# Kernel tuning notes

Measured on AMD Instinct MI355X. Metric: run time of the kernel, lower is better.

## Reference

```python
import jax, jax.numpy as jnp
import numpy as np

NUM_BINS_X = 1024
NUM_BINS_Y = 1024
XL, XH, YL, YH = 0.0, 1024.0, 0.0, 1024.0
NUM_NODES = 4_000_000
NUM_FILLER = 1_000_000
NUM_PHYS = NUM_NODES - NUM_FILLER      # physical = movable + fixed
NUM_MOVABLE = 2_500_000
UNIT_PIN_CAPACITY = 2.0                # pins per unit area capacity
PIN_STRETCH_RATIO = 1.414              # DREAMPlace default sqrt(2)
MAX_ADJ = 2.5
MIN_ADJ = 1.0 / MAX_ADJ
SPAN = 4                               # max bins any box spans per axis (sizes <= 2*bin)


def setup_inputs() -> dict:
    key = jax.random.key(0)
    k1, k2, k3, k4, k5 = jax.random.split(key, 5)
    node_size_x = 0.5 + 1.5 * jax.random.uniform(k1, (NUM_NODES,), jnp.float32)
    node_size_y = 0.5 + 1.5 * jax.random.uniform(k2, (NUM_NODES,), jnp.float32)
    pos_x = XL + jax.random.uniform(k3, (NUM_NODES,), jnp.float32) * (XH - XL - 2.0)
    pos_y = YL + jax.random.uniform(k4, (NUM_NODES,), jnp.float32) * (YH - YL - 2.0)
    pos = jnp.concatenate([pos_x, pos_y])  # [2*num_nodes], x then y
    pin_weights = jax.random.randint(k5, (NUM_PHYS,), 1, 9, jnp.int32)
    return {"pos": pos, "node_size_x": node_size_x, "node_size_y": node_size_y,
            "pin_weights": pin_weights}


def _overlap(lo, hi, bin_lo, bin_size):
    # overlap length of interval [lo,hi] with bin [bin_lo, bin_lo+bin_size]
    return jnp.clip(jnp.minimum(hi, bin_lo + bin_size) - jnp.maximum(lo, bin_lo), 0.0, None)


def reference(pos, node_size_x, node_size_y, pin_weights):
    bsx = (XH - XL) / NUM_BINS_X
    bsy = (YH - YL) / NUM_BINS_Y
    dtype = pos.dtype

    # ---- phase 1: pin density map over stretched boxes of physical nodes ----
    sx = node_size_x[:NUM_PHYS]
    sy = node_size_y[:NUM_PHYS]
    hx = 0.5 * jnp.maximum(bsx * PIN_STRETCH_RATIO, sx)  # half stretched extent
    hy = 0.5 * jnp.maximum(bsy * PIN_STRETCH_RATIO, sy)
    cx = pos[:NUM_PHYS] + 0.5 * sx
    cy = pos[NUM_NODES:NUM_NODES + NUM_PHYS] + 0.5 * sy
    xmin, xmax = cx - hx, cx + hx
    ymin, ymax = cy - hy, cy + hy
    dens = pin_weights.astype(dtype) / (4.0 * hx * hy)   # pins per unit area

    bxl = jnp.clip(jnp.floor((xmin - XL) / bsx).astype(jnp.int32), 0, NUM_BINS_X - 1)
    byl = jnp.clip(jnp.floor((ymin - YL) / bsy).astype(jnp.int32), 0, NUM_BINS_Y - 1)

    pmap = jnp.zeros(NUM_BINS_X * NUM_BINS_Y, dtype)
    for di in range(SPAN):
        bx = bxl + di
        ox = _overlap(xmin, xmax, XL + bx.astype(dtype) * bsx, bsx)
        vx = bx < NUM_BINS_X
        for dj in range(SPAN):
            by = byl + dj
            oy = _overlap(ymin, ymax, YL + by.astype(dtype) * bsy, bsy)
            v = vx & (by < NUM_BINS_Y)
            idx = jnp.where(v, bx * NUM_BINS_Y + by, 0)
            val = jnp.where(v, dens * ox * oy, 0.0)
            pmap = pmap.at[idx].add(val)

    # density -> utilization: scatter added pins*overlap/area, divide by bin area
    pmap = pmap / (bsx * bsy)
    adj = jnp.clip(pmap / UNIT_PIN_CAPACITY, MIN_ADJ, MAX_ADJ)

    # ---- phase 2: per-movable-node pin-optimized area over actual footprint ----
    mx = pos[:NUM_MOVABLE]
    my = pos[NUM_NODES:NUM_NODES + NUM_MOVABLE]
    msx = node_size_x[:NUM_MOVABLE]
    msy = node_size_y[:NUM_MOVABLE]
    bxl2 = jnp.clip(jnp.floor((mx - XL) / bsx).astype(jnp.int32), 0, NUM_BINS_X - 1)
    byl2 = jnp.clip(jnp.floor((my - YL) / bsy).astype(jnp.int32), 0, NUM_BINS_Y - 1)

    area = jnp.zeros(NUM_MOVABLE, dtype)
    for di in range(SPAN):
        bx = bxl2 + di
        ox = _overlap(mx, mx + msx, XL + bx.astype(dtype) * bsx, bsx)
        vx = bx < NUM_BINS_X
        for dj in range(SPAN):
            by = byl2 + dj
            oy = _overlap(my, my + msy, YL + by.astype(dtype) * bsy, bsy)
            v = vx & (by < NUM_BINS_Y)
            idx = jnp.where(v, bx * NUM_BINS_Y + by, 0)
            area = area + jnp.where(v, ox * oy * adj[idx], 0.0)
    return area
```

## Files before the change

### kernel.cpp

```cpp
#include <hip/hip_runtime.h>

#define NBX 1024
#define NBY 1024
#define TS 64
#define NTX (NBX / TS)
#define NTY (NBY / TS)
#define NTILES (NTX * NTY)
#define LW 66
#define LSTRIDE 67
#define CAP 13056
#define CAPM 11008

#define FB_BLOCK 512
#define FB_K 8
#define FB_CHUNK (FB_BLOCK * FB_K)

#define SPLIT 2

#define PMAP_SCALE 131072.0f
#define PMAP_INV   (1.0f / 131072.0f)

static constexpr int NUM_NODES   = 4000000;
static constexpr int NUM_PHYS    = 3000000;
static constexpr int NUM_MOVABLE = 2500000;
static constexpr int HALF_MOV    = NUM_MOVABLE / 2;

typedef unsigned long long u64;

static constexpr size_t OFF_PMAP  = 0;
static constexpr size_t OFF_CURS  = OFF_PMAP + (size_t)NBX * NBY * 4;
static constexpr size_t OFF_CURSM = OFF_CURS + NTILES * 4;
static constexpr size_t OFF_SLAB  = ((OFF_CURSM + NTILES * 4 + 15) / 16) * 16;
static constexpr size_t OFF_MSLAB = ((OFF_SLAB + (size_t)NTILES * CAP * 8 + 15) / 16) * 16;
static constexpr size_t WS_FULL   = OFF_MSLAB + (size_t)NTILES * CAPM * 12;

__global__ void __launch_bounds__(FB_BLOCK)
fill_both(const float* __restrict__ pos, const float* __restrict__ nsx,
          const float* __restrict__ nsy, const int* __restrict__ pw,
          unsigned* __restrict__ curs, unsigned* __restrict__ cursm,
          uint2* __restrict__ slab, uint3* __restrict__ mslab) {
    __shared__ unsigned cntp[NTILES], cntm[NTILES];
    __shared__ unsigned offp[NTILES], offm[NTILES];
    __shared__ unsigned Dp[NTILES], Dm[NTILES];
    __shared__ unsigned wsum[8];
    __shared__ uint2 SAB[FB_CHUNK];
    __shared__ unsigned SC[FB_CHUNK];
    __shared__ unsigned short ST[FB_CHUNK];

    const int tid = threadIdx.x;
    const int b0  = blockIdx.x * FB_CHUNK;

    if (tid < NTILES) { cntp[tid] = 0u; cntm[tid] = 0u; }
    __syncthreads();

    u64 P[FB_K];
    u64 M[FB_K];
    int TPM[FB_K];
    unsigned rkP[FB_K], rkM[FB_K];

    #pragma unroll
    for (int k = 0; k < FB_K; ++k) {
        int i = b0 + k * FB_BLOCK + tid;
        int tp = -1, tm = -1;
        if (i < NUM_PHYS) {
            float mx = pos[i], my = pos[NUM_NODES + i];
            float sx = nsx[i], sy = nsy[i];
            float hx = 0.5f * fmaxf(1.414f, sx);
            float hy = 0.5f * fmaxf(1.414f, sy);
            unsigned qhx = (unsigned)__float2int_rn((hx - 0.7f) * 1024.0f);
            unsigned qhy = (unsigned)__float2int_rn((hy - 0.7f) * 1024.0f);
            float hxd = 0.7f + (float)qhx * (1.0f / 1024.0f);
            float hyd = 0.7f + (float)qhy * (1.0f / 1024.0f);
            float xmin = mx + 0.5f * sx - hxd;
            float ymin = my + 0.5f * sy - hyd;
            int bxl = min(max((int)floorf(xmin), 0), NBX - 1);
            int byl = min(max((int)floorf(ymin), 0), NBY - 1);
            tp = (bxl >> 6) * NTY + (byl >> 6);
            int bx0 = (tp >> 4) << 6, by0 = (tp & 15) << 6;
            unsigned ex = (unsigned)__float2int_rn((xmin - (float)bx0 + 1.0f) * 8192.0f);
            unsigned ey = (unsigned)__float2int_rn((ymin - (float)by0 + 1.0f) * 8192.0f);
            P[k] = (u64)ex | ((u64)ey << 20) | ((u64)qhx << 40)
                 | ((u64)qhy << 50) | ((u64)(unsigned)(pw[i] - 1) << 60);
            rkP[k] = atomicAdd(&cntp[tp], 1u);
            if (i < NUM_MOVABLE) {
                int bxm = min(max((int)floorf(mx), 0), NBX - 1);
                int bym = min(max((int)floorf(my), 0), NBY - 1);
                tm = (bxm >> 6) * NTY + (bym >> 6);
                int bx0m = (tm >> 4) << 6, by0m = (tm & 15) << 6;
                unsigned exm = (unsigned)__float2int_rn((mx - (float)bx0m) * 8192.0f);
                unsigned eym = (unsigned)__float2int_rn((my - (float)by0m) * 8192.0f);
                unsigned qsx = (unsigned)__float2int_rn((sx - 0.5f) * 2048.0f);
                unsigned qsy = (unsigned)__float2int_rn((sy - 0.5f) * 2048.0f);
                M[k] = (u64)exm | ((u64)eym << 20) | ((u64)qsx << 40) | ((u64)qsy << 52);
                rkM[k] = atomicAdd(&cntm[tm], 1u);
            }
        }
        TPM[k] = (tp & 0xffff) | (tm << 16);
    }
    __syncthreads();

    {
        const int lane   = tid & 63;
        const int scanId = tid & 255;
        const bool isMov = tid >= 256;
        unsigned* cnt = isMov ? cntm : cntp;
        unsigned* off = isMov ? offm : offp;
        unsigned* D   = isMov ? Dm : Dp;
        unsigned* gc  = isMov ? cursm : curs;

        unsigned v = cnt[scanId];
        unsigned x = v;
        #pragma unroll
        for (int d = 1; d < 64; d <<= 1) {
            unsigned y = __shfl_up(x, d);
            if (lane >= d) x += y;
        }
        if (lane == 63) wsum[tid >> 6] = x;
        __syncthreads();
        unsigned add = 0;
        const int w0  = isMov ? 4 : 0;
        const int myw = scanId >> 6;
        for (int w = 0; w < myw; ++w) add += wsum[w0 + w];
        unsigned o = x + add - v;
        unsigned base = v ? atomicAdd(&gc[scanId], v) : 0u;
        off[scanId] = o;
        D[scanId]   = base - o;
    }
    __syncthreads();

    #pragma unroll
    for (int k = 0; k < FB_K; ++k) {
        int tp = (int)(short)(TPM[k] & 0xffff);
        if (tp >= 0) {
            unsigned s = offp[tp] + rkP[k];
            SAB[s] = make_uint2((unsigned)P[k], (unsigned)(P[k] >> 32));
            ST[s]  = (unsigned short)tp;
        }
    }
    __syncthreads();

    {
        unsigned totP = offp[NTILES - 1] + cntp[NTILES - 1];
        for (unsigned j = tid; j < totP; j += FB_BLOCK) {
            unsigned tile = ST[j];
            unsigned p = Dp[tile] + j;
            if (p < CAP)
                slab[(size_t)tile * CAP + p] = SAB[j];
        }
    }
    __syncthreads();

    #pragma unroll
    for (int k = 0; k < FB_K; ++k) {
        int tm = TPM[k] >> 16;
        if (tm >= 0) {
            unsigned s = offm[tm] + rkM[k];
            SAB[s] = make_uint2((unsigned)M[k], (unsigned)(M[k] >> 32));
            SC[s]  = (unsigned)(b0 + k * FB_BLOCK + tid);
            ST[s]  = (unsigned short)tm;
        }
    }
    __syncthreads();

    {
        unsigned totM = offm[NTILES - 1] + cntm[NTILES - 1];
        for (unsigned j = tid; j < totM; j += FB_BLOCK) {
            unsigned tile = ST[j];
            unsigned p = Dm[tile] + j;
            if (p < CAPM) {
                uint2 ab = SAB[j];
                mslab[(size_t)tile * CAPM + p] = make_uint3(ab.x, ab.y, SC[j]);
            }
        }
    }
}

__global__ void __launch_bounds__(1024)
tile_scatter(const uint2* __restrict__ slab, const unsigned* __restrict__ curs,
             float* __restrict__ pmap) {
    __shared__ unsigned lds[LW * LSTRIDE];
    int t   = blockIdx.x / SPLIT;
    int sub = blockIdx.x - t * SPLIT;
    int bx0 = (t >> 4) << 6, by0 = (t & 15) << 6;

    for (int c = threadIdx.x; c < LW * LSTRIDE; c += 1024) lds[c] = 0u;
    __syncthreads();

    unsigned n = min(curs[t], (unsigned)CAP);
    const uint2* sl = slab + (size_t)t * CAP;

    unsigned k = threadIdx.x + sub * 1024;
    uint2 p = (k < n) ? sl[k] : make_uint2(0u, 0u);
    while (k < n) {
        unsigned kn = k + SPLIT * 1024;
        uint2 pn = (kn < n) ? sl[kn] : make_uint2(0u, 0u);

        u64 P = (u64)p.x | ((u64)p.y << 32);
        float xminl = (float)(P & 0xFFFFFu)         * (1.0f / 8192.0f) - 1.0f;
        float yminl = (float)((P >> 20) & 0xFFFFFu) * (1.0f / 8192.0f) - 1.0f;
        float hx = 0.7f + (float)((P >> 40) & 0x3FFu) * (1.0f / 1024.0f);
        float hy = 0.7f + (float)((P >> 50) & 0x3FFu) * (1.0f / 1024.0f);
        float pwv  = (float)(1u + (unsigned)(P >> 60));
        float dens = pwv / (4.0f * hx * hy);
        float xmaxl = xminl + 2.0f * hx;
        float ymaxl = yminl + 2.0f * hy;

        int lx0 = min(max((int)floorf(xminl), 0), TS - 1);
        int ly0 = min(max((int)floorf(yminl), 0), TS - 1);
        #pragma unroll
        for (int di = 0; di < 3; ++di) {
            float bl = (float)(lx0 + di);
            float ox = fminf(xmaxl, bl + 1.0f) - fmaxf(xminl, bl);
            if (ox <= 0.0f) continue;
            float dox = dens * ox;
            #pragma unroll
            for (int dj = 0; dj < 3; ++dj) {
                float bly = (float)(ly0 + dj);
                float oy  = fminf(ymaxl, bly + 1.0f) - fmaxf(yminl, bly);
                if (oy > 0.0f) {
                    unsigned q = (unsigned)__float2int_rn(dox * oy * PMAP_SCALE);
                    atomicAdd(&lds[(lx0 + di) * LSTRIDE + (ly0 + dj)], q);
                }
            }
        }
        p = pn;
        k = kn;
    }
    __syncthreads();

    for (int c = threadIdx.x; c < LW * LW; c += 1024) {
        int lx = c / LW, ly = c - lx * LW;
        int bx = bx0 + lx, by = by0 + ly;
        if (bx >= NBX || by >= NBY) continue;
        float v = (float)lds[lx * LSTRIDE + ly] * PMAP_INV;
        if (v != 0.0f)
            atomicAdd(&pmap[bx * NBY + by], v);
    }
}

__global__ void __launch_bounds__(1024)
gather_tile(const uint3* __restrict__ mslab, const unsigned* __restrict__ cursm,
            const float* __restrict__ pmap, float* __restrict__ out) {
    __shared__ float adj[LW * LSTRIDE];
    int t   = blockIdx.x / SPLIT;
    int sub = blockIdx.x - t * SPLIT;
    int bx0 = (t >> 4) << 6, by0 = (t & 15) << 6;

    for (int c = threadIdx.x; c < LW * LW; c += 1024) {
        int r = c / LW, col = c - r * LW;
        int bx = min(bx0 + r,  NBX - 1);
        int by = min(by0 + col, NBY - 1);
        adj[r * LSTRIDE + col] =
            fminf(fmaxf(pmap[bx * NBY + by] * 0.5f, 0.4f), 2.5f);
    }
    __syncthreads();

    unsigned n = min(cursm[t], (unsigned)CAPM);
    const uint3* sl = mslab + (size_t)t * CAPM;

    for (unsigned k = threadIdx.x + sub * 1024; k < n; k += SPLIT * 1024) {
        uint3 p = sl[k];
        u64 M = (u64)p.x | ((u64)p.y << 32);
        float mxl = (float)(M & 0xFFFFFu)         * (1.0f / 8192.0f);
        float myl = (float)((M >> 20) & 0xFFFFFu) * (1.0f / 8192.0f);
        float sx  = 0.5f + (float)((M >> 40) & 0xFFFu) * (1.0f / 2048.0f);
        float sy  = 0.5f + (float)(M >> 52)            * (1.0f / 2048.0f);
        float xmaxl = mxl + sx;
        float ymaxl = myl + sy;

        int lx0 = min((int)mxl, TS - 1);
        int ly0 = min((int)myl, TS - 1);

        float area = 0.0f;
        #pragma unroll
        for (int di = 0; di < 3; ++di) {
            float bl = (float)(lx0 + di);
            float ox = fmaxf(fminf(xmaxl, bl + 1.0f) - fmaxf(mxl, bl), 0.0f);
            #pragma unroll
            for (int dj = 0; dj < 3; ++dj) {
                float bly = (float)(ly0 + dj);
                float oy  = fmaxf(fminf(ymaxl, bly + 1.0f) - fmaxf(myl, bly), 0.0f);
                area += ox * oy * adj[(lx0 + di) * LSTRIDE + (ly0 + dj)];
            }
        }
        out[p.z] = area;
    }
}

__global__ void __launch_bounds__(256)
scatter_pin(const float* __restrict__ pos, const float* __restrict__ nsx,
            const float* __restrict__ nsy, const int* __restrict__ pw,
            float* __restrict__ pmap) {
    int i = blockIdx.x * blockDim.x + threadIdx.x;
    if (i >= NUM_PHYS) return;
    float sx = nsx[i], sy = nsy[i];
    float hx = 0.5f * fmaxf(1.414f, sx);
    float hy = 0.5f * fmaxf(1.414f, sy);
    float cx = pos[i] + 0.5f * sx;
    float cy = pos[NUM_NODES + i] + 0.5f * sy;
    float xmin = cx - hx, xmax = cx + hx;
    float ymin = cy - hy, ymax = cy + hy;
    float dens = (float)pw[i] / (4.0f * hx * hy);
    int bxl = min(max((int)floorf(xmin), 0), NBX - 1);
    int byl = min(max((int)floorf(ymin), 0), NBY - 1);
    #pragma unroll
    for (int di = 0; di < 3; ++di) {
        float bl = (float)(bxl + di);
        float ox = fminf(xmax, bl + 1.0f) - fmaxf(xmin, bl);
        if (ox <= 0.0f) continue;
        float dox = dens * ox;
        int base = min(bxl + di, NBX - 1) * NBY;
        #pragma unroll
        for (int dj = 0; dj < 3; ++dj) {
            float bly = (float)(byl + dj);
            float oy  = fminf(ymax, bly + 1.0f) - fmaxf(ymin, bly);
            if (oy > 0.0f) atomicAdd(&pmap[base + min(byl + dj, NBY - 1)], dox * oy);
        }
    }
}

__device__ __forceinline__ float gather_one(const float* __restrict__ pos,
                                            const float* __restrict__ nsx,
                                            const float* __restrict__ nsy,
                                            const float* __restrict__ pmap,
                                            int i) {
    float mx = pos[i];
    float my = pos[NUM_NODES + i];
    float xmax = mx + nsx[i];
    float ymax = my + nsy[i];
    int bxl = min(max((int)floorf(mx), 0), NBX - 1);
    int byl = min(max((int)floorf(my), 0), NBY - 1);
    float ox[3], oy[3];
    int rowb[3], colb[3];
    #pragma unroll
    for (int d = 0; d < 3; ++d) {
        float bl  = (float)(bxl + d);
        float bly = (float)(byl + d);
        ox[d] = fmaxf(fminf(xmax, bl + 1.0f) - fmaxf(mx, bl), 0.0f);
        oy[d] = fmaxf(fminf(ymax, bly + 1.0f) - fmaxf(my, bly), 0.0f);
        rowb[d] = min(bxl + d, NBX - 1) * NBY;
        colb[d] = min(byl + d, NBY - 1);
    }
    float area = 0.0f;
    #pragma unroll
    for (int di = 0; di < 3; ++di)
        #pragma unroll
        for (int dj = 0; dj < 3; ++dj) {
            float a = fminf(fmaxf(pmap[rowb[di] + colb[dj]] * 0.5f, 0.4f), 2.5f);
            area += ox[di] * oy[dj] * a;
        }
    return area;
}

__global__ void __launch_bounds__(256)
gather_area(const float* __restrict__ pos, const float* __restrict__ nsx,
            const float* __restrict__ nsy, const float* __restrict__ pmap,
            float* __restrict__ out) {
    int i = blockIdx.x * blockDim.x + threadIdx.x;
    if (i >= HALF_MOV) return;
    int i2 = i + HALF_MOV;
    float a1 = gather_one(pos, nsx, nsy, pmap, i);
    float a2 = gather_one(pos, nsx, nsy, pmap, i2);
    out[i]  = a1;
    out[i2] = a2;
}

extern "C" void kernel_launch(void* const* d_in, const int* in_sizes, int n_in,
                              void* d_out, int out_size, void* d_ws, size_t ws_size,
                              hipStream_t stream) {
    const float* pos = (const float*)d_in[0];
    const float* nsx = (const float*)d_in[1];
    const float* nsy = (const float*)d_in[2];
    const int*   pw  = (const int*)d_in[3];
    float* out = (float*)d_out;

    char* ws = (char*)d_ws;
    float*    pmap  = (float*)(ws + OFF_PMAP);
    unsigned* curs  = (unsigned*)(ws + OFF_CURS);
    unsigned* cursm = (unsigned*)(ws + OFF_CURSM);
    uint2*    slab  = (uint2*)(ws + OFF_SLAB);
    uint3*    mslab = (uint3*)(ws + OFF_MSLAB);

    if (ws_size >= WS_FULL) {
        hipMemsetAsync(ws, 0, OFF_SLAB, stream);
        int grid = (NUM_PHYS + FB_CHUNK - 1) / FB_CHUNK;
        fill_both   <<<grid, FB_BLOCK, 0, stream>>>(pos, nsx, nsy, pw,
                                                    curs, cursm, slab, mslab);
        tile_scatter<<<NTILES * SPLIT, 1024, 0, stream>>>(slab, curs, pmap);
        gather_tile <<<NTILES * SPLIT, 1024, 0, stream>>>(mslab, cursm, pmap, out);
    } else {
        hipMemsetAsync(pmap, 0, (size_t)NBX * NBY * sizeof(float), stream);
        scatter_pin <<<(NUM_PHYS + 255) / 256, 256, 0, stream>>>(pos, nsx, nsy, pw, pmap);
        gather_area <<<(HALF_MOV + 255) / 256, 256, 0, stream>>>(pos, nsx, nsy, pmap, out);
    }
}
```

Measured before the change: 182.2 us.

## Fuse binning, tile scatter and gather into one cooperative persistent kernel

Replaces the three kernel launches with one cooperative kernel of 512 blocks. Blocks pull binning chunks from an atomic work counter, then use grid.sync to separate the tile scatter phase from the gather phase, with a shared-memory union reused across phases. Block size changes to 1024 threads with 4 items each. The aim is to remove launch gaps and tail imbalance. In exchange, the grid size is tied to 512 tiles-times-split, the shared-memory union may limit occupancy in the binning phase, and the code falls back to the slow path if the cooperative launch fails.

```diff
diff --git a/kernel.cpp b/kernel.cpp
--- a/kernel.cpp
+++ b/kernel.cpp
@@ -1,4 +1,7 @@
 #include <hip/hip_runtime.h>
+#include <hip/hip_cooperative_groups.h>
+
+namespace cg = cooperative_groups;
 
 #define NBX 1024
 #define NBY 1024
@@ -11,10 +14,12 @@
 #define CAP 13056
 #define CAPM 11008
 
-#define FB_BLOCK 512
-#define FB_K 8
+#define FB_BLOCK 1024
+#define FB_K 4
 #define FB_CHUNK (FB_BLOCK * FB_K)
-
+#define NCHUNKS ((3000000 + FB_CHUNK - 1) / FB_CHUNK)
+
+#define FUSE_GRID 512
 #define SPLIT 2
 
 #define PMAP_SCALE 131072.0f
@@ -30,260 +35,277 @@
 static constexpr size_t OFF_PMAP  = 0;
 static constexpr size_t OFF_CURS  = OFF_PMAP + (size_t)NBX * NBY * 4;
 static constexpr size_t OFF_CURSM = OFF_CURS + NTILES * 4;
-static constexpr size_t OFF_SLAB  = ((OFF_CURSM + NTILES * 4 + 15) / 16) * 16;
+static constexpr size_t OFF_WORK  = OFF_CURSM + NTILES * 4;
+static constexpr size_t OFF_SLAB  = ((OFF_WORK + 4 + 15) / 16) * 16;
 static constexpr size_t OFF_MSLAB = ((OFF_SLAB + (size_t)NTILES * CAP * 8 + 15) / 16) * 16;
 static constexpr size_t WS_FULL   = OFF_MSLAB + (size_t)NTILES * CAPM * 12;
 
-__global__ void __launch_bounds__(FB_BLOCK)
-fill_both(const float* __restrict__ pos, const float* __restrict__ nsx,
+__global__ void __launch_bounds__(FB_BLOCK, 8)
+fused_all(const float* __restrict__ pos, const float* __restrict__ nsx,
           const float* __restrict__ nsy, const int* __restrict__ pw,
           unsigned* __restrict__ curs, unsigned* __restrict__ cursm,
-          uint2* __restrict__ slab, uint3* __restrict__ mslab) {
-    __shared__ unsigned cntp[NTILES], cntm[NTILES];
-    __shared__ unsigned offp[NTILES], offm[NTILES];
-    __shared__ unsigned Dp[NTILES], Dm[NTILES];
-    __shared__ unsigned wsum[8];
-    __shared__ uint2 SAB[FB_CHUNK];
-    __shared__ unsigned SC[FB_CHUNK];
-    __shared__ unsigned short ST[FB_CHUNK];
+          unsigned* __restrict__ work,
+          uint2* __restrict__ slab, uint3* __restrict__ mslab,
+          float* __restrict__ pmap, float* __restrict__ out) {
+    cg::grid_group grid = cg::this_grid();
+
+    __shared__ union {
+        struct {
+            unsigned cntp[NTILES], cntm[NTILES];
+            unsigned offp[NTILES], offm[NTILES];
+            unsigned Dp[NTILES], Dm[NTILES];
+            unsigned wsum[8];
+            uint2 SAB[FB_CHUNK];
+            unsigned SC[FB_CHUNK];
+            unsigned short ST[FB_CHUNK];
+        } a;
+        unsigned acc[LW * LSTRIDE];
+        float    adj[LW * LSTRIDE];
+    } sh;
+    __shared__ unsigned chunkId;
 
     const int tid = threadIdx.x;
-    const int b0  = blockIdx.x * FB_CHUNK;
-
-    if (tid < NTILES) { cntp[tid] = 0u; cntm[tid] = 0u; }
-    __syncthreads();
-
-    u64 P[FB_K];
-    u64 M[FB_K];
-    int TPM[FB_K];
-    unsigned rkP[FB_K], rkM[FB_K];
-
-    #pragma unroll
-    for (int k = 0; k < FB_K; ++k) {
-        int i = b0 + k * FB_BLOCK + tid;
-        int tp = -1, tm = -1;
-        if (i < NUM_PHYS) {
-            float mx = pos[i], my = pos[NUM_NODES + i];
-            float sx = nsx[i], sy = nsy[i];
-            float hx = 0.5f * fmaxf(1.414f, sx);
-            float hy = 0.5f * fmaxf(1.414f, sy);
-            unsigned qhx = (unsigned)__float2int_rn((hx - 0.7f) * 1024.0f);
-            unsigned qhy = (unsigned)__float2int_rn((hy - 0.7f) * 1024.0f);
-            float hxd = 0.7f + (float)qhx * (1.0f / 1024.0f);
-            float hyd = 0.7f + (float)qhy * (1.0f / 1024.0f);
-            float xmin = mx + 0.5f * sx - hxd;
-            float ymin = my + 0.5f * sy - hyd;
-            int bxl = min(max((int)floorf(xmin), 0), NBX - 1);
-            int byl = min(max((int)floorf(ymin), 0), NBY - 1);
-            tp = (bxl >> 6) * NTY + (byl >> 6);
-            int bx0 = (tp >> 4) << 6, by0 = (tp & 15) << 6;
-            unsigned ex = (unsigned)__float2int_rn((xmin - (float)bx0 + 1.0f) * 8192.0f);
-            unsigned ey = (unsigned)__float2int_rn((ymin - (float)by0 + 1.0f) * 8192.0f);
-            P[k] = (u64)ex | ((u64)ey << 20) | ((u64)qhx << 40)
-                 | ((u64)qhy << 50) | ((u64)(unsigned)(pw[i] - 1) << 60);
-            rkP[k] = atomicAdd(&cntp[tp], 1u);
-            if (i < NUM_MOVABLE) {
-                int bxm = min(max((int)floorf(mx), 0), NBX - 1);
-                int bym = min(max((int)floorf(my), 0), NBY - 1);
-                tm = (bxm >> 6) * NTY + (bym >> 6);
-                int bx0m = (tm >> 4) << 6, by0m = (tm & 15) << 6;
-                unsigned exm = (unsigned)__float2int_rn((mx - (float)bx0m) * 8192.0f);
-                unsigned eym = (unsigned)__float2int_rn((my - (float)by0m) * 8192.0f);
-                unsigned qsx = (unsigned)__float2int_rn((sx - 0.5f) * 2048.0f);
-                unsigned qsy = (unsigned)__float2int_rn((sy - 0.5f) * 2048.0f);
-                M[k] = (u64)exm | ((u64)eym << 20) | ((u64)qsx << 40) | ((u64)qsy << 52);
-                rkM[k] = atomicAdd(&cntm[tm], 1u);
-            }
-        }
-        TPM[k] = (tp & 0xffff) | (tm << 16);
-    }
-    __syncthreads();
+
+    for (;;) {
+        if (tid == 0) chunkId = atomicAdd(work, 1u);
+        if (tid < NTILES) { sh.a.cntp[tid] = 0u; sh.a.cntm[tid] = 0u; }
+        __syncthreads();
+        const unsigned c = chunkId;
+        if (c >= NCHUNKS) break;
+        const int b0 = (int)c * FB_CHUNK;
+
+        u64 P[FB_K];
+        u64 M[FB_K];
+        int TPM[FB_K];
+        unsigned rkP[FB_K], rkM[FB_K];
+
+        #pragma unroll
+        for (int k = 0; k < FB_K; ++k) {
+            int i = b0 + k * FB_BLOCK + tid;
+            int tp = -1, tm = -1;
+            if (i < NUM_PHYS) {
+                float mx = pos[i], my = pos[NUM_NODES + i];
+                float sx = nsx[i], sy = nsy[i];
+                float hx = 0.5f * fmaxf(1.414f, sx);
+                float hy = 0.5f * fmaxf(1.414f, sy);
+                unsigned qhx = (unsigned)__float2int_rn((hx - 0.7f) * 1024.0f);
+                unsigned qhy = (unsigned)__float2int_rn((hy - 0.7f) * 1024.0f);
+                float hxd = 0.7f + (float)qhx * (1.0f / 1024.0f);
+                float hyd = 0.7f + (float)qhy * (1.0f / 1024.0f);
+                float xmin = mx + 0.5f * sx - hxd;
+                float ymin = my + 0.5f * sy - hyd;
+                int bxl = min(max((int)floorf(xmin), 0), NBX - 1);
+                int byl = min(max((int)floorf(ymin), 0), NBY - 1);
+                tp = (bxl >> 6) * NTY + (byl >> 6);
+                int bx0 = (tp >> 4) << 6, by0 = (tp & 15) << 6;
+                unsigned ex = (unsigned)__float2int_rn((xmin - (float)bx0 + 1.0f) * 8192.0f);
+                unsigned ey = (unsigned)__float2int_rn((ymin - (float)by0 + 1.0f) * 8192.0f);
+                P[k] = (u64)ex | ((u64)ey << 20) | ((u64)qhx << 40)
+                     | ((u64)qhy << 50) | ((u64)(unsigned)(pw[i] - 1) << 60);
+                rkP[k] = atomicAdd(&sh.a.cntp[tp], 1u);
+                if (i < NUM_MOVABLE) {
+                    int bxm = min(max((int)floorf(mx), 0), NBX - 1);
+                    int bym = min(max((int)floorf(my), 0), NBY - 1);
+                    tm = (bxm >> 6) * NTY + (bym >> 6);
+                    int bx0m = (tm >> 4) << 6, by0m = (tm & 15) << 6;
+                    unsigned exm = (unsigned)__float2int_rn((mx - (float)bx0m) * 8192.0f);
+                    unsigned eym = (unsigned)__float2int_rn((my - (float)by0m) * 8192.0f);
+                    unsigned qsx = (unsigned)__float2int_rn((sx - 0.5f) * 2048.0f);
+                    unsigned qsy = (unsigned)__float2int_rn((sy - 0.5f) * 2048.0f);
+                    M[k] = (u64)exm | ((u64)eym << 20) | ((u64)qsx << 40) | ((u64)qsy << 52);
+                    rkM[k] = atomicAdd(&sh.a.cntm[tm], 1u);
+                }
+            }
+            TPM[k] = (tp & 0xffff) | (tm << 16);
+        }
+        __syncthreads();
+
+        unsigned v = 0, x = 0;
+        if (tid < 512) {
+            const int lane = tid & 63;
+            const int scanId = tid & 255;
+            v = (tid >= 256) ? sh.a.cntm[scanId] : sh.a.cntp[scanId];
+            x = v;
+            #pragma unroll
+            for (int d = 1; d < 64; d <<= 1) {
+                unsigned y = __shfl_up(x, d);
+                if (lane >= d) x += y;
+            }
+            if (lane == 63) sh.a.wsum[tid >> 6] = x;
+        }
+        __syncthreads();
+        if (tid < 512) {
+            const int scanId = tid & 255;
+            const bool isMov = tid >= 256;
+            unsigned add = 0;
+            const int w0 = isMov ? 4 : 0;
+            for (int w = 0; w < (scanId >> 6); ++w) add += sh.a.wsum[w0 + w];
+            unsigned o = x + add - v;
+            unsigned* gc = isMov ? cursm : curs;
+            unsigned base = v ? atomicAdd(&gc[scanId], v) : 0u;
+            if (isMov) { sh.a.offm[scanId] = o; sh.a.Dm[scanId] = base - o; }
+            else       { sh.a.offp[scanId] = o; sh.a.Dp[scanId] = base - o; }
+        }
+        __syncthreads();
+
+        #pragma unroll
+        for (int k = 0; k < FB_K; ++k) {
+            int tp = (int)(short)(TPM[k] & 0xffff);
+            if (tp >= 0) {
+                unsigned s = sh.a.offp[tp] + rkP[k];
+                sh.a.SAB[s] = make_uint2((unsigned)P[k], (unsigned)(P[k] >> 32));
+                sh.a.ST[s]  = (unsigned short)tp;
+            }
+        }
+        __syncthreads();
+
+        {
+            unsigned tot = sh.a.offp[NTILES - 1] + sh.a.cntp[NTILES - 1];
+            for (unsigned j = tid; j < tot; j += FB_BLOCK) {
+                unsigned tile = sh.a.ST[j];
+                unsigned p = sh.a.Dp[tile] + j;
+                if (p < CAP)
+                    slab[(size_t)tile * CAP + p] = sh.a.SAB[j];
+            }
+        }
+        __syncthreads();
+
+        #pragma unroll
+        for (int k = 0; k < FB_K; ++k) {
+            int tm = TPM[k] >> 16;
+            if (tm >= 0) {
+                unsigned s = sh.a.offm[tm] + rkM[k];
+                sh.a.SAB[s] = make_uint2((unsigned)M[k], (unsigned)(M[k] >> 32));
+                sh.a.SC[s]  = (unsigned)(b0 + k * FB_BLOCK + tid);
+                sh.a.ST[s]  = (unsigned short)tm;
+            }
+        }
+        __syncthreads();
+
+        {
+            unsigned tot = sh.a.offm[NTILES - 1] + sh.a.cntm[NTILES - 1];
+            for (unsigned j = tid; j < tot; j += FB_BLOCK) {
+                unsigned tile = sh.a.ST[j];
+                unsigned p = sh.a.Dm[tile] + j;
+                if (p < CAPM) {
+                    uint2 ab = sh.a.SAB[j];
+                    mslab[(size_t)tile * CAPM + p] = make_uint3(ab.x, ab.y, sh.a.SC[j]);
+                }
+            }
+        }
+        __syncthreads();
+    }
+
+    __threadfence();
+    grid.sync();
 
     {
-        const int lane   = tid & 63;
-        const int scanId = tid & 255;
-        const bool isMov = tid >= 256;
-        unsigned* cnt = isMov ? cntm : cntp;
-        unsigned* off = isMov ? offm : offp;
-        unsigned* D   = isMov ? Dm : Dp;
-        unsigned* gc  = isMov ? cursm : curs;
-
-        unsigned v = cnt[scanId];
-        unsigned x = v;
-        #pragma unroll
-        for (int d = 1; d < 64; d <<= 1) {
-            unsigned y = __shfl_up(x, d);
-            if (lane >= d) x += y;
-        }
-        if (lane == 63) wsum[tid >> 6] = x;
-        __syncthreads();
-        unsigned add = 0;
-        const int w0  = isMov ? 4 : 0;
-        const int myw = scanId >> 6;
-        for (int w = 0; w < myw; ++w) add += wsum[w0 + w];
-        unsigned o = x + add - v;
-        unsigned base = v ? atomicAdd(&gc[scanId], v) : 0u;
-        off[scanId] = o;
-        D[scanId]   = base - o;
-    }
-    __syncthreads();
-
-    #pragma unroll
-    for (int k = 0; k < FB_K; ++k) {
-        int tp = (int)(short)(TPM[k] & 0xffff);
-        if (tp >= 0) {
-            unsigned s = offp[tp] + rkP[k];
-            SAB[s] = make_uint2((unsigned)P[k], (unsigned)(P[k] >> 32));
-            ST[s]  = (unsigned short)tp;
-        }
-    }
-    __syncthreads();
+        int t   = blockIdx.x / SPLIT;
+        int sub = blockIdx.x - t * SPLIT;
+        int bx0 = (t >> 4) << 6, by0 = (t & 15) << 6;
+
+        for (int cix = tid; cix < LW * LSTRIDE; cix += FB_BLOCK) sh.acc[cix] = 0u;
+        __syncthreads();
+
+        unsigned n = min(curs[t], (unsigned)CAP);
+        const uint2* sl = slab + (size_t)t * CAP;
+
+        unsigned k = tid + sub * FB_BLOCK;
+        uint2 p = (k < n) ? sl[k] : make_uint2(0u, 0u);
+        while (k < n) {
+            unsigned kn = k + SPLIT * FB_BLOCK;
+            uint2 pn = (kn < n) ? sl[kn] : make_uint2(0u, 0u);
+
+            u64 P = (u64)p.x | ((u64)p.y << 32);
+            float xminl = (float)(P & 0xFFFFFu)         * (1.0f / 8192.0f) - 1.0f;
+            float yminl = (float)((P >> 20) & 0xFFFFFu) * (1.0f / 8192.0f) - 1.0f;
+            float hx = 0.7f + (float)((P >> 40) & 0x3FFu) * (1.0f / 1024.0f);
+            float hy = 0.7f + (float)((P >> 50) & 0x3FFu) * (1.0f / 1024.0f);
+            float pwv  = (float)(1u + (unsigned)(P >> 60));
+            float dens = pwv / (4.0f * hx * hy);
+            float xmaxl = xminl + 2.0f * hx;
+            float ymaxl = yminl + 2.0f * hy;
+
+            int lx0 = min(max((int)floorf(xminl), 0), TS - 1);
+            int ly0 = min(max((int)floorf(yminl), 0), TS - 1);
+            #pragma unroll
+            for (int di = 0; di < 3; ++di) {
+                float bl = (float)(lx0 + di);
+                float ox = fminf(xmaxl, bl + 1.0f) - fmaxf(xminl, bl);
+                if (ox <= 0.0f) continue;
+                float dox = dens * ox;
+                #pragma unroll
+                for (int dj = 0; dj < 3; ++dj) {
+                    float bly = (float)(ly0 + dj);
+                    float oy  = fminf(ymaxl, bly + 1.0f) - fmaxf(yminl, bly);
+                    if (oy > 0.0f) {
+                        unsigned q = (unsigned)__float2int_rn(dox * oy * PMAP_SCALE);
+                        atomicAdd(&sh.acc[(lx0 + di) * LSTRIDE + (ly0 + dj)], q);
+                    }
+                }
+            }
+            p = pn;
+            k = kn;
+        }
+        __syncthreads();
+
+        for (int cix = tid; cix < LW * LW; cix += FB_BLOCK) {
+            int lx = cix / LW, ly = cix - lx * LW;
+            int bx = bx0 + lx, by = by0 + ly;
+            if (bx >= NBX || by >= NBY) continue;
+            float vv = (float)sh.acc[lx * LSTRIDE + ly] * PMAP_INV;
+            if (vv != 0.0f)
+                atomicAdd(&pmap[bx * NBY + by], vv);
+        }
+    }
+
+    __threadfence();
+    grid.sync();
 
     {
-        unsigned totP = offp[NTILES - 1] + cntp[NTILES - 1];
-        for (unsigned j = tid; j < totP; j += FB_BLOCK) {
-            unsigned tile = ST[j];
-            unsigned p = Dp[tile] + j;
-            if (p < CAP)
-                slab[(size_t)tile * CAP + p] = SAB[j];
-        }
-    }
-    __syncthreads();
-
-    #pragma unroll
-    for (int k = 0; k < FB_K; ++k) {
-        int tm = TPM[k] >> 16;
-        if (tm >= 0) {
-            unsigned s = offm[tm] + rkM[k];
-            SAB[s] = make_uint2((unsigned)M[k], (unsigned)(M[k] >> 32));
-            SC[s]  = (unsigned)(b0 + k * FB_BLOCK + tid);
-            ST[s]  = (unsigned short)tm;
-        }
-    }
-    __syncthreads();
-
-    {
-        unsigned totM = offm[NTILES - 1] + cntm[NTILES - 1];
-        for (unsigned j = tid; j < totM; j += FB_BLOCK) {
-            unsigned tile = ST[j];
-            unsigned p = Dm[tile] + j;
-            if (p < CAPM) {
-                uint2 ab = SAB[j];
-                mslab[(size_t)tile * CAPM + p] = make_uint3(ab.x, ab.y, SC[j]);
-            }
-        }
-    }
-}
-
-__global__ void __launch_bounds__(1024)
-tile_scatter(const uint2* __restrict__ slab, const unsigned* __restrict__ curs,
-             float* __restrict__ pmap) {
-    __shared__ unsigned lds[LW * LSTRIDE];
-    int t   = blockIdx.x / SPLIT;
-    int sub = blockIdx.x - t * SPLIT;
-    int bx0 = (t >> 4) << 6, by0 = (t & 15) << 6;
-
-    for (int c = threadIdx.x; c < LW * LSTRIDE; c += 1024) lds[c] = 0u;
-    __syncthreads();
-
-    unsigned n = min(curs[t], (unsigned)CAP);
-    const uint2* sl = slab + (size_t)t * CAP;
-
-    unsigned k = threadIdx.x + sub * 1024;
-    uint2 p = (k < n) ? sl[k] : make_uint2(0u, 0u);
-    while (k < n) {
-        unsigned kn = k + SPLIT * 1024;
-        uint2 pn = (kn < n) ? sl[kn] : make_uint2(0u, 0u);
-
-        u64 P = (u64)p.x | ((u64)p.y << 32);
-        float xminl = (float)(P & 0xFFFFFu)         * (1.0f / 8192.0f) - 1.0f;
-        float yminl = (float)((P >> 20) & 0xFFFFFu) * (1.0f / 8192.0f) - 1.0f;
-        float hx = 0.7f + (float)((P >> 40) & 0x3FFu) * (1.0f / 1024.0f);
-        float hy = 0.7f + (float)((P >> 50) & 0x3FFu) * (1.0f / 1024.0f);
-        float pwv  = (float)(1u + (unsigned)(P >> 60));
-        float dens = pwv / (4.0f * hx * hy);
-        float xmaxl = xminl + 2.0f * hx;
-        float ymaxl = yminl + 2.0f * hy;
-
-        int lx0 = min(max((int)floorf(xminl), 0), TS - 1);
-        int ly0 = min(max((int)floorf(yminl), 0), TS - 1);
-        #pragma unroll
-        for (int di = 0; di < 3; ++di) {
-            float bl = (float)(lx0 + di);
-            float ox = fminf(xmaxl, bl + 1.0f) - fmaxf(xminl, bl);
-            if (ox <= 0.0f) continue;
-            float dox = dens * ox;
+        int t   = blockIdx.x / SPLIT;
+        int sub = blockIdx.x - t * SPLIT;
+        int bx0 = (t >> 4) << 6, by0 = (t & 15) << 6;
+
+        for (int cix = tid; cix < LW * LW; cix += FB_BLOCK) {
+            int r = cix / LW, col = cix - r * LW;
+            int bx = min(bx0 + r,  NBX - 1);
+            int by = min(by0 + col, NBY - 1);
+            sh.adj[r * LSTRIDE + col] =
+                fminf(fmaxf(pmap[bx * NBY + by] * 0.5f, 0.4f), 2.5f);
+        }
+        __syncthreads();
+
+        unsigned n = min(cursm[t], (unsigned)CAPM);
+        const uint3* sl = mslab + (size_t)t * CAPM;
+
+        for (unsigned k = tid + sub * FB_BLOCK; k < n; k += SPLIT * FB_BLOCK) {
+            uint3 p = sl[k];
+            u64 M = (u64)p.x | ((u64)p.y << 32);
+            float mxl = (float)(M & 0xFFFFFu)         * (1.0f / 8192.0f);
+            float myl = (float)((M >> 20) & 0xFFFFFu) * (1.0f / 8192.0f);
+            float sx  = 0.5f + (float)((M >> 40) & 0xFFFu) * (1.0f / 2048.0f);
+            float sy  = 0.5f + (float)(M >> 52)            * (1.0f / 2048.0f);
+            float xmaxl = mxl + sx;
+            float ymaxl = myl + sy;
+
+            int lx0 = min((int)mxl, TS - 1);
+            int ly0 = min((int)myl, TS - 1);
+
+            float area = 0.0f;
             #pragma unroll
-            for (int dj = 0; dj < 3; ++dj) {
-                float bly = (float)(ly0 + dj);
-                float oy  = fminf(ymaxl, bly + 1.0f) - fmaxf(yminl, bly);
-                if (oy > 0.0f) {
-                    unsigned q = (unsigned)__float2int_rn(dox * oy * PMAP_SCALE);
-                    atomicAdd(&lds[(lx0 + di) * LSTRIDE + (ly0 + dj)], q);
+            for (int di = 0; di < 3; ++di) {
+                float bl = (float)(lx0 + di);
+                float ox = fmaxf(fminf(xmaxl, bl + 1.0f) - fmaxf(mxl, bl), 0.0f);
+                #pragma unroll
+                for (int dj = 0; dj < 3; ++dj) {
+                    float bly = (float)(ly0 + dj);
+                    float oy  = fmaxf(fminf(ymaxl, bly + 1.0f) - fmaxf(myl, bly), 0.0f);
+                    area += ox * oy * sh.adj[(lx0 + di) * LSTRIDE + (ly0 + dj)];
                 }
             }
-        }
-        p = pn;
-        k = kn;
-    }
-    __syncthreads();
-
-    for (int c = threadIdx.x; c < LW * LW; c += 1024) {
-        int lx = c / LW, ly = c - lx * LW;
-        int bx = bx0 + lx, by = by0 + ly;
-        if (bx >= NBX || by >= NBY) continue;
-        float v = (float)lds[lx * LSTRIDE + ly] * PMAP_INV;
-        if (v != 0.0f)
-            atomicAdd(&pmap[bx * NBY + by], v);
-    }
-}
-
-__global__ void __launch_bounds__(1024)
-gather_tile(const uint3* __restrict__ mslab, const unsigned* __restrict__ cursm,
-            const float* __restrict__ pmap, float* __restrict__ out) {
-    __shared__ float adj[LW * LSTRIDE];
-    int t   = blockIdx.x / SPLIT;
-    int sub = blockIdx.x - t * SPLIT;
-    int bx0 = (t >> 4) << 6, by0 = (t & 15) << 6;
-
-    for (int c = threadIdx.x; c < LW * LW; c += 1024) {
-        int r = c / LW, col = c - r * LW;
-        int bx = min(bx0 + r,  NBX - 1);
-        int by = min(by0 + col, NBY - 1);
-        adj[r * LSTRIDE + col] =
-            fminf(fmaxf(pmap[bx * NBY + by] * 0.5f, 0.4f), 2.5f);
-    }
-    __syncthreads();
-
-    unsigned n = min(cursm[t], (unsigned)CAPM);
-    const uint3* sl = mslab + (size_t)t * CAPM;
-
-    for (unsigned k = threadIdx.x + sub * 1024; k < n; k += SPLIT * 1024) {
-        uint3 p = sl[k];
-        u64 M = (u64)p.x | ((u64)p.y << 32);
-        float mxl = (float)(M & 0xFFFFFu)         * (1.0f / 8192.0f);
-        float myl = (float)((M >> 20) & 0xFFFFFu) * (1.0f / 8192.0f);
-        float sx  = 0.5f + (float)((M >> 40) & 0xFFFu) * (1.0f / 2048.0f);
-        float sy  = 0.5f + (float)(M >> 52)            * (1.0f / 2048.0f);
-        float xmaxl = mxl + sx;
-        float ymaxl = myl + sy;
-
-        int lx0 = min((int)mxl, TS - 1);
-        int ly0 = min((int)myl, TS - 1);
-
-        float area = 0.0f;
-        #pragma unroll
-        for (int di = 0; di < 3; ++di) {
-            float bl = (float)(lx0 + di);
-            float ox = fmaxf(fminf(xmaxl, bl + 1.0f) - fmaxf(mxl, bl), 0.0f);
-            #pragma unroll
-            for (int dj = 0; dj < 3; ++dj) {
-                float bly = (float)(ly0 + dj);
-                float oy  = fmaxf(fminf(ymaxl, bly + 1.0f) - fmaxf(myl, bly), 0.0f);
-                area += ox * oy * adj[(lx0 + di) * LSTRIDE + (ly0 + dj)];
-            }
-        }
-        out[p.z] = area;
+            out[p.z] = area;
+        }
     }
 }
 
@@ -378,17 +400,22 @@
     float*    pmap  = (float*)(ws + OFF_PMAP);
     unsigned* curs  = (unsigned*)(ws + OFF_CURS);
     unsigned* cursm = (unsigned*)(ws + OFF_CURSM);
+    unsigned* work  = (unsigned*)(ws + OFF_WORK);
     uint2*    slab  = (uint2*)(ws + OFF_SLAB);
     uint3*    mslab = (uint3*)(ws + OFF_MSLAB);
 
+    bool ok = false;
     if (ws_size >= WS_FULL) {
         hipMemsetAsync(ws, 0, OFF_SLAB, stream);
-        int grid = (NUM_PHYS + FB_CHUNK - 1) / FB_CHUNK;
-        fill_both   <<<grid, FB_BLOCK, 0, stream>>>(pos, nsx, nsy, pw,
-                                                    curs, cursm, slab, mslab);
-        tile_scatter<<<NTILES * SPLIT, 1024, 0, stream>>>(slab, curs, pmap);
-        gather_tile <<<NTILES * SPLIT, 1024, 0, stream>>>(mslab, cursm, pmap, out);
-    } else {
+        void* args[] = {(void*)&pos, (void*)&nsx, (void*)&nsy, (void*)&pw,
+                        (void*)&curs, (void*)&cursm, (void*)&work,
+                        (void*)&slab, (void*)&mslab, (void*)&pmap, (void*)&out};
+        hipError_t e = hipLaunchCooperativeKernel((void*)fused_all,
+                                                  dim3(FUSE_GRID), dim3(FB_BLOCK),
+                                                  args, 0, stream);
+        ok = (e == hipSuccess);
+    }
+    if (!ok) {
         hipMemsetAsync(pmap, 0, (size_t)NBX * NBY * sizeof(float), stream);
         scatter_pin <<<(NUM_PHYS + 255) / 256, 256, 0, stream>>>(pos, nsx, nsy, pw, pmap);
         gather_area <<<(HALF_MOV + 255) / 256, 256, 0, stream>>>(pos, nsx, nsy, pmap, out);
```

Result: slower. 621.7 us (+241.2%).
